# Optimization experiments

Hardware: AMD Instinct MI355X
Metric: run time of the kernel (lower is better)

## Reference

```python
import jax, jax.numpy as jnp
import numpy as np

# Model config (mirrors Mamba2Block(dim=256) with mamba_ssm defaults)
D_MODEL = 256
EXPAND = 2
D_INNER = D_MODEL * EXPAND          # 512
HEADDIM = D_MODEL * EXPAND // 8     # 64
NHEADS = D_INNER // HEADDIM         # 8
D_STATE = 64
D_CONV = 4
CONV_DIM = D_INNER + 2 * D_STATE    # 640 (ngroups=1)
D_IN_PROJ = 2 * D_INNER + 2 * D_STATE + NHEADS  # 1160
BATCH, SEQLEN = 2, 2048
EPS = 1e-5


def setup_inputs() -> dict:
    key = jax.random.key(0)
    ks = jax.random.split(key, 12)
    s = 0.02
    return {
        "hidden_states": jax.random.normal(ks[0], (BATCH, SEQLEN, D_MODEL), jnp.float32),
        "norm_w": jnp.ones((D_MODEL,), jnp.float32),
        "norm_b": jnp.zeros((D_MODEL,), jnp.float32),
        "W_in": jax.random.normal(ks[1], (D_MODEL, D_IN_PROJ), jnp.float32) * s,
        "conv_w": jax.random.normal(ks[2], (CONV_DIM, D_CONV), jnp.float32) * 0.25,
        "conv_b": jnp.zeros((CONV_DIM,), jnp.float32),
        "dt_bias": jax.random.uniform(ks[3], (NHEADS,), jnp.float32),
        "A_log": jax.random.uniform(ks[4], (NHEADS,), jnp.float32),  # A = -exp(A_log) in (-e, -1]
        "D_param": jnp.ones((NHEADS,), jnp.float32),
        "rms_w": jnp.ones((D_INNER,), jnp.float32),
        "W_out": jax.random.normal(ks[5], (D_INNER, D_MODEL), jnp.float32) * s,
    }


def _layer_norm(x, w, b):
    mu = jnp.mean(x, -1, keepdims=True)
    var = jnp.mean((x - mu) ** 2, -1, keepdims=True)
    return (x - mu) * jax.lax.rsqrt(var + EPS) * w + b


def _causal_depthwise_conv(x, w, b):
    # x: [B,L,C], w: [C,K] depthwise causal conv
    B, L, C = x.shape
    K = w.shape[1]
    xp = jnp.pad(x, ((0, 0), (K - 1, 0), (0, 0)))
    y = b
    for k in range(K):  # K=4, fixed small kernel
        y = y + w[:, k] * xp[:, k:k + L, :]
    return y


def reference(hidden_states, norm_w, norm_b, W_in, conv_w, conv_b, dt_bias, A_log, D_param, rms_w, W_out):
    B, L, D = hidden_states.shape
    residual = hidden_states                       # residual is None, drop_path=0
    x = _layer_norm(residual, norm_w, norm_b)      # pre-norm

    zxbcdt = jnp.einsum("bld,de->ble", x, W_in)    # [B,L,2*Di+2*N+H]
    z = zxbcdt[..., :D_INNER]
    xBC = zxbcdt[..., D_INNER:D_INNER + CONV_DIM]
    dt = zxbcdt[..., -NHEADS:]

    xBC = jax.nn.silu(_causal_depthwise_conv(xBC, conv_w, conv_b))
    xs = xBC[..., :D_INNER]
    Bm = xBC[..., D_INNER:D_INNER + D_STATE]       # [B,L,N] (ngroups=1)
    Cm = xBC[..., D_INNER + D_STATE:]              # [B,L,N]

    dt = jax.nn.softplus(dt + dt_bias)             # [B,L,H]
    A = -jnp.exp(A_log)                            # [H]
    dA = jnp.exp(dt * A)                           # [B,L,H]

    xh = xs.reshape(B, L, NHEADS, HEADDIM)         # [B,L,H,P]
    dtx = dt[..., None] * xh                       # [B,L,H,P]

    def step(s, inp):
        dA_t, dtx_t, B_t, C_t = inp                # [B,H],[B,H,P],[B,N],[B,N]
        s = s * dA_t[:, :, None, None] + dtx_t[..., None] * B_t[:, None, None, :]
        y_t = jnp.einsum("bhpn,bn->bhp", s, C_t)
        return s, y_t

    s0 = jnp.zeros((B, NHEADS, HEADDIM, D_STATE), hidden_states.dtype)
    xs_in = (jnp.swapaxes(dA, 0, 1), jnp.swapaxes(dtx, 0, 1),
             jnp.swapaxes(Bm, 0, 1), jnp.swapaxes(Cm, 0, 1))
    _, ys = jax.lax.scan(step, s0, xs_in)          # ys: [L,B,H,P]
    y = jnp.swapaxes(ys, 0, 1) + D_param[None, None, :, None] * xh  # skip term
    y = y.reshape(B, L, D_INNER)

    # gated RMSNorm (norm_before_gate=False): rmsnorm(y * silu(z)) * rms_w
    g = y * jax.nn.silu(z)
    g = g * jax.lax.rsqrt(jnp.mean(g * g, -1, keepdims=True) + EPS) * rms_w

    out = jnp.einsum("bld,de->ble", g, W_out)
    return out, residual
```

## Files before the change

### kernel.cpp

```cpp
#include <hip/hip_runtime.h>
#include <hip/hip_bf16.h>

#define BATCH 2
#define SEQLEN 2048
#define DMODEL 256
#define DINNER 512
#define NHEADS 8
#define HEADDIM 64
#define DSTATE 64
#define CONVDIM 640
#define DINPROJ 1160
#define NTOK (BATCH*SEQLEN)
#define Q 64
#define NCH (SEQLEN/Q)
#define NPAD_IN 1216
#define TS 72

typedef short v8s __attribute__((ext_vector_type(8)));
typedef float v4f __attribute__((ext_vector_type(4)));

__device__ __forceinline__ unsigned short f2bf(float f){
    __hip_bfloat16 h = __float2bfloat16(f);
    return *reinterpret_cast<unsigned short*>(&h);
}
__device__ __forceinline__ float bf2f(unsigned short u){
    unsigned int x = ((unsigned int)u) << 16;
    return __uint_as_float(x);
}

__global__ __launch_bounds__(256) void k_prep(
        const float* __restrict__ hid, const float* __restrict__ nw, const float* __restrict__ nb,
        const float* __restrict__ Win, const float* __restrict__ Wout,
        float* __restrict__ res, unsigned short* __restrict__ Xb,
        unsigned short* __restrict__ Wti, unsigned short* __restrict__ Wto){
    int bx = blockIdx.x;
    int t = threadIdx.x;
    if(bx < 256){
        __shared__ float xs[16][DMODEL];
        int tok0 = bx*16;
        for(int i=0;i<16;i++){
            int idx = i*256+t; int j = idx>>8, c = idx&255;
            float v = hid[(size_t)(tok0+j)*DMODEL + c];
            xs[j][c] = v;
            res[(size_t)(tok0+j)*DMODEL + c] = v;
        }
        __syncthreads();
        int g = t>>4, il = t&15;
        float sum=0.f, sumsq=0.f;
        for(int i=0;i<16;i++){ float v = xs[g][il*16+i]; sum += v; sumsq += v*v; }
        #pragma unroll
        for(int m=1;m<16;m<<=1){ sum += __shfl_xor(sum,m); sumsq += __shfl_xor(sumsq,m); }
        float mu   = sum*(1.f/256.f);
        float var  = sumsq*(1.f/256.f) - mu*mu;
        float rstd = rsqrtf(var + 1e-5f);
        for(int i=0;i<16;i++){
            int c = il*16+i;
            xs[g][c] = (xs[g][c]-mu)*rstd*nw[c] + nb[c];
        }
        __syncthreads();
        for(int i=0;i<16;i++){
            int idx = i*256+t; int j = idx>>8, c = idx&255;
            Xb[(size_t)(tok0+j)*DMODEL + c] = f2bf(xs[j][c]);
        }
    } else if(bx < 256 + NPAD_IN/4){
        int n0 = (bx-256)*4, k = t;
        #pragma unroll
        for(int i=0;i<4;i++){
            int n = n0+i;
            float v = (n < DINPROJ) ? Win[(size_t)k*DINPROJ + n] : 0.f;
            Wti[(size_t)n*DMODEL + k] = f2bf(v);
        }
    } else {
        int n0 = (bx - 256 - NPAD_IN/4)*4;
        #pragma unroll
        for(int kk=0;kk<2;kk++){
            int k = t + kk*256;
            #pragma unroll
            for(int i=0;i<4;i++){
                int n = n0+i;
                Wto[(size_t)n*DINNER + k] = f2bf(Wout[(size_t)k*DMODEL + n]);
            }
        }
    }
}

template<int BF16OUT>
__global__ __launch_bounds__(256) void k_gemm(
        const unsigned short* __restrict__ A, const unsigned short* __restrict__ Bt,
        float* __restrict__ Cf, unsigned short* __restrict__ Cb, int K, int Ncols){
    __shared__ __align__(16) unsigned short As[128*40];
    __shared__ __align__(16) unsigned short Bs[64*40];
    int t = threadIdx.x;
    int lane = t & 63, w = t >> 6;
    int lanelow = lane & 15, quad = lane >> 4;
    int tok0 = blockIdx.x * 128;
    int n0   = blockIdx.y * 64;
    v4f acc[2][4];
    #pragma unroll
    for(int mi=0;mi<2;mi++)
        #pragma unroll
        for(int ni=0;ni<4;ni++)
            acc[mi][ni] = (v4f){0.f,0.f,0.f,0.f};
    for(int k0=0; k0<K; k0+=32){
        __syncthreads();
        #pragma unroll
        for(int cc=0; cc<2; cc++){
            int c = t + cc*256;
            int row = c>>2, off = c&3;
            uint4 v = *(const uint4*)(A + (size_t)(tok0+row)*K + k0 + off*8);
            *(uint4*)&As[row*40 + off*8] = v;
        }
        {
            int row = t>>2, off = t&3;
            uint4 v = *(const uint4*)(Bt + (size_t)(n0+row)*K + k0 + off*8);
            *(uint4*)&Bs[row*40 + off*8] = v;
        }
        __syncthreads();
        v8s a0 = *(const v8s*)&As[(w*32 +      lanelow)*40 + quad*8];
        v8s a1 = *(const v8s*)&As[(w*32 + 16 + lanelow)*40 + quad*8];
        v8s b[4];
        #pragma unroll
        for(int ni=0;ni<4;ni++)
            b[ni] = *(const v8s*)&Bs[(ni*16 + lanelow)*40 + quad*8];
        #pragma unroll
        for(int ni=0;ni<4;ni++){
            acc[0][ni] = __builtin_amdgcn_mfma_f32_16x16x32_bf16(a0, b[ni], acc[0][ni], 0,0,0);
            acc[1][ni] = __builtin_amdgcn_mfma_f32_16x16x32_bf16(a1, b[ni], acc[1][ni], 0,0,0);
        }
    }
    #pragma unroll
    for(int mi=0;mi<2;mi++){
        #pragma unroll
        for(int ni=0;ni<4;ni++){
            int col = n0 + ni*16 + lanelow;
            if(col < Ncols){
                #pragma unroll
                for(int r=0;r<4;r++){
                    int row = tok0 + w*32 + mi*16 + quad*4 + r;
                    if(BF16OUT) Cb[(size_t)row*Ncols + col] = f2bf(acc[mi][ni][r]);
                    else        Cf[(size_t)row*Ncols + col] = acc[mi][ni][r];
                }
            }
        }
    }
}

__global__ __launch_bounds__(256) void k_chunk1(
        const unsigned short* __restrict__ zxb, const float* __restrict__ conv_w, const float* __restrict__ conv_b,
        const float* __restrict__ dt_bias, const float* __restrict__ A_log, const float* __restrict__ D_param,
        unsigned short* __restrict__ yw16, float* __restrict__ contrib,
        float* __restrict__ Larr, float* __restrict__ decayArr, unsigned short* __restrict__ Ccv){
    int blk = blockIdx.x;
    int c = blk & 31, h = (blk>>5)&7, b = blk>>8;
    int t = threadIdx.x;
    int lane = t & 63, w = t >> 6;
    int lanelow = lane & 15, quad = lane >> 4;
    __shared__ __align__(16) unsigned short Cb[64*TS];
    __shared__ __align__(16) unsigned short Bb[64*TS];
    __shared__ __align__(16) unsigned short BtW[64*TS];
    __shared__ __align__(16) unsigned short Xt[64*TS];
    __shared__ __align__(16) unsigned short Gbuf[64*TS];
    __shared__ float Ls[Q], dts[Q], wch[Q];
    int l0 = c*Q;
    int bh = b*NHEADS + h;
    const unsigned short* zbase = zxb + (size_t)(b*SEQLEN + l0)*DINPROJ;
    if(t < Q){
        float v = bf2f(zbase[(size_t)t*DINPROJ + (DINPROJ-NHEADS) + h]) + dt_bias[h];
        float dt = (v > 20.f) ? v : log1pf(__expf(v));
        float A  = -__expf(A_log[h]);
        float ld = dt*A;
        #pragma unroll
        for(int off=1; off<64; off<<=1){
            float u = __shfl_up(ld, off);
            if(lane >= off) ld += u;
        }
        Ls[t] = ld; dts[t] = dt;
    }
    __syncthreads();
    float L63 = Ls[Q-1];
    if(t < Q) wch[t] = __expf(L63 - Ls[t]) * dts[t];
    __syncthreads();
    unsigned short* CcP = Ccv + ((size_t)b*NCH + c)*4096;
    for(int i=0;i<12;i++){
        int u = t + 256*i;
        int st = u & 63, c4 = u >> 6, ch = c4*4;
        int gcol = (ch < 64) ? (DINNER + h*HEADDIM + ch) : (2*DINNER + (ch-64));
        const unsigned short* colp = zbase + (ptrdiff_t)st*DINPROJ + gcol;
        float xk[4][4];
        #pragma unroll
        for(int k=0;k<4;k++){
            int l = l0 + st + k - 3;
            ushort4 v;
            if(l >= 0) v = *(const ushort4*)(colp - (ptrdiff_t)(3-k)*DINPROJ);
            else { v.x=0; v.y=0; v.z=0; v.w=0; }
            xk[k][0]=bf2f(v.x); xk[k][1]=bf2f(v.y); xk[k][2]=bf2f(v.z); xk[k][3]=bf2f(v.w);
        }
        float wst = wch[st];
        #pragma unroll
        for(int j=0;j<4;j++){
            int chj = ch+j;
            int cc = (chj<64) ? (h*HEADDIM + chj) : (448 + chj);
            float4 wv = *(const float4*)&conv_w[cc*4];
            float acc = conv_b[cc] + wv.x*xk[0][j] + wv.y*xk[1][j] + wv.z*xk[2][j] + wv.w*xk[3][j];
            float sv = acc/(1.f+__expf(-acc));
            if(chj < 64){
                Xt[chj*TS + st] = f2bf(sv);
            } else if(chj < 128){
                int n = chj-64;
                Bb[st*TS + n]  = f2bf(sv);
                BtW[n*TS + st] = f2bf(sv*wst);
            } else {
                int n = chj-128;
                unsigned short sb = f2bf(sv);
                Cb[st*TS + n] = sb;
                if(h==0) CcP[st*64 + n] = sb;
            }
        }
    }
    __syncthreads();
    v4f g[4];
    #pragma unroll
    for(int nt=0;nt<4;nt++) g[nt] = (v4f){0.f,0.f,0.f,0.f};
    #pragma unroll
    for(int kk=0;kk<2;kk++){
        v8s a = *(const v8s*)&Cb[(w*16+lanelow)*TS + kk*32 + quad*8];
        #pragma unroll
        for(int nt=0;nt<4;nt++){
            v8s bb = *(const v8s*)&Bb[(nt*16+lanelow)*TS + kk*32 + quad*8];
            g[nt] = __builtin_amdgcn_mfma_f32_16x16x32_bf16(a, bb, g[nt], 0,0,0);
        }
    }
    float Lrow[4];
    #pragma unroll
    for(int r=0;r<4;r++) Lrow[r] = Ls[w*16 + quad*4 + r];
    #pragma unroll
    for(int nt=0;nt<4;nt++){
        int col = nt*16 + lanelow;
        float Lc = Ls[col], dtc = dts[col];
        #pragma unroll
        for(int r=0;r<4;r++){
            int rowg = w*16 + quad*4 + r;
            float val = (col <= rowg) ? g[nt][r] * __expf(Lrow[r]-Lc) * dtc : 0.f;
            Gbuf[rowg*TS + col] = f2bf(val);
        }
    }
    __syncthreads();
    v4f ya[4], sa[4];
    #pragma unroll
    for(int nt=0;nt<4;nt++){ ya[nt]=(v4f){0.f,0.f,0.f,0.f}; sa[nt]=(v4f){0.f,0.f,0.f,0.f}; }
    #pragma unroll
    for(int kk=0;kk<2;kk++){
        v8s ag = *(const v8s*)&Gbuf[(w*16+lanelow)*TS + kk*32 + quad*8];
        v8s ax = *(const v8s*)&Xt[(w*16+lanelow)*TS + kk*32 + quad*8];
        #pragma unroll
        for(int nt=0;nt<4;nt++){
            v8s bx = *(const v8s*)&Xt[(nt*16+lanelow)*TS + kk*32 + quad*8];
            v8s bw = *(const v8s*)&BtW[(nt*16+lanelow)*TS + kk*32 + quad*8];
            ya[nt] = __builtin_amdgcn_mfma_f32_16x16x32_bf16(ag, bx, ya[nt], 0,0,0);
            sa[nt] = __builtin_amdgcn_mfma_f32_16x16x32_bf16(ax, bw, sa[nt], 0,0,0);
        }
    }
    float Dp = D_param[h];
    #pragma unroll
    for(int nt=0;nt<4;nt++){
        int col = nt*16 + lanelow;
        #pragma unroll
        for(int r=0;r<4;r++){
            int i = w*16 + quad*4 + r;
            float xval = bf2f(Xt[col*TS + i]);
            yw16[((size_t)b*SEQLEN + l0 + i)*DINNER + h*HEADDIM + col] = f2bf(ya[nt][r] + Dp*xval);
            contrib[(((size_t)bh*NCH + c)*64 + i)*64 + col] = sa[nt][r];
        }
    }
    if(t < Q) Larr[((size_t)bh*NCH + c)*Q + t] = Ls[t];
    if(t == 0) decayArr[bh*NCH + c] = __expf(L63);
}

__global__ __launch_bounds__(256) void k_chunk2(const float* __restrict__ contrib,
                                                const float* __restrict__ decayArr,
                                                unsigned short* __restrict__ Sb){
    int bh = blockIdx.x >> 4;
    int part = blockIdx.x & 15;
    int e = part*256 + threadIdx.x;
    const size_t base = (size_t)bh*NCH*4096 + e;
    float vals[NCH];
    #pragma unroll
    for(int c=0;c<NCH;c++) vals[c] = contrib[base + (size_t)c*4096];
    float s = 0.f;
    #pragma unroll
    for(int c=0;c<NCH;c++){
        Sb[base + (size_t)c*4096] = f2bf(s);
        s = fmaf(s, decayArr[bh*NCH + c], vals[c]);
    }
}

__global__ __launch_bounds__(512) void k_tail(
        const unsigned short* __restrict__ Ccv, const unsigned short* __restrict__ Sb,
        const float* __restrict__ Larr, const unsigned short* __restrict__ yw16,
        const unsigned short* __restrict__ zxb, const float* __restrict__ rms_w,
        unsigned short* __restrict__ Gb){
    int blk = blockIdx.x;
    int half = blk & 1, c = (blk>>1) & 31, b = blk >> 6;
    int t = threadIdx.x;
    int h = t >> 6, lane = t & 63;
    int lanelow = lane & 15, quad = lane >> 4;
    int bh = b*NHEADS + h;
    __shared__ float wsum[8][32];
    __shared__ float rstdS[32];
    const unsigned short* Cp = Ccv + ((size_t)b*NCH + c)*4096;
    const unsigned short* Sp = Sb + ((size_t)bh*NCH + c)*4096;
    v8s a[2][2];
    #pragma unroll
    for(int rt=0;rt<2;rt++){
        int row = half*32 + rt*16 + lanelow;
        a[rt][0] = *(const v8s*)(Cp + row*64 + quad*8);
        a[rt][1] = *(const v8s*)(Cp + row*64 + 32 + quad*8);
    }
    v8s s[4][2];
    #pragma unroll
    for(int nt=0;nt<4;nt++){
        s[nt][0] = *(const v8s*)(Sp + (nt*16+lanelow)*64 + quad*8);
        s[nt][1] = *(const v8s*)(Sp + (nt*16+lanelow)*64 + 32 + quad*8);
    }
    float g[2][4][4];
    float sq[2][4];
    const float* Lp = Larr + ((size_t)bh*NCH + c)*Q;
    #pragma unroll
    for(int rt=0;rt<2;rt++){
        float eL[4];
        #pragma unroll
        for(int r=0;r<4;r++) eL[r] = __expf(Lp[half*32 + rt*16 + quad*4 + r]);
        #pragma unroll
        for(int nt=0;nt<4;nt++){
            v4f acc = (v4f){0.f,0.f,0.f,0.f};
            acc = __builtin_amdgcn_mfma_f32_16x16x32_bf16(a[rt][0], s[nt][0], acc, 0,0,0);
            acc = __builtin_amdgcn_mfma_f32_16x16x32_bf16(a[rt][1], s[nt][1], acc, 0,0,0);
            int col = h*HEADDIM + nt*16 + lanelow;
            #pragma unroll
            for(int r=0;r<4;r++){
                int i = half*32 + rt*16 + quad*4 + r;
                size_t tok = (size_t)b*SEQLEN + c*Q + i;
                float yv = acc[r]*eL[r] + bf2f(yw16[tok*DINNER + col]);
                float z  = bf2f(zxb[tok*DINPROJ + col]);
                float gg = yv * (z/(1.f+__expf(-z)));
                g[rt][nt][r] = gg;
                sq[rt][r] = (nt==0 ? gg*gg : sq[rt][r] + gg*gg);
            }
        }
    }
    #pragma unroll
    for(int rt=0;rt<2;rt++)
        #pragma unroll
        for(int r=0;r<4;r++){
            float v = sq[rt][r];
            #pragma unroll
            for(int m=1;m<16;m<<=1) v += __shfl_xor(v, m);
            sq[rt][r] = v;
        }
    if(lanelow==0){
        #pragma unroll
        for(int rt=0;rt<2;rt++)
            #pragma unroll
            for(int r=0;r<4;r++)
                wsum[h][rt*16 + quad*4 + r] = sq[rt][r];
    }
    __syncthreads();
    if(t < 32){
        float tot = 0.f;
        #pragma unroll
        for(int hh=0;hh<8;hh++) tot += wsum[hh][t];
        rstdS[t] = rsqrtf(tot*(1.f/512.f) + 1e-5f);
    }
    __syncthreads();
    #pragma unroll
    for(int rt=0;rt<2;rt++){
        #pragma unroll
        for(int nt=0;nt<4;nt++){
            int col = h*HEADDIM + nt*16 + lanelow;
            float rw = rms_w[col];
            #pragma unroll
            for(int r=0;r<4;r++){
                int i = rt*16 + quad*4 + r;
                Gb[((size_t)b*SEQLEN + c*Q + half*32 + i)*DINNER + col] = f2bf(g[rt][nt][r] * rstdS[i] * rw);
            }
        }
    }
}

extern "C" void kernel_launch(void* const* d_in, const int* in_sizes, int n_in,
                              void* d_out, int out_size, void* d_ws, size_t ws_size,
                              hipStream_t stream) {
    const float* hid     = (const float*)d_in[0];
    const float* norm_w  = (const float*)d_in[1];
    const float* norm_b  = (const float*)d_in[2];
    const float* Win     = (const float*)d_in[3];
    const float* conv_w  = (const float*)d_in[4];
    const float* conv_b  = (const float*)d_in[5];
    const float* dt_bias = (const float*)d_in[6];
    const float* A_log   = (const float*)d_in[7];
    const float* D_param = (const float*)d_in[8];
    const float* rms_w   = (const float*)d_in[9];
    const float* Wout    = (const float*)d_in[10];

    float* ws = (float*)d_ws;
    float* contrib = ws;
    float* Larr    = contrib + (size_t)16*NCH*4096;
    float* decayA  = Larr + (size_t)16*NCH*Q;
    unsigned short* zxb  = (unsigned short*)(decayA + 512);
    unsigned short* yw16 = zxb + (size_t)NTOK*DINPROJ;
    unsigned short* Sb   = yw16 + (size_t)NTOK*DINNER;
    unsigned short* Ccv  = Sb + (size_t)16*NCH*4096;
    unsigned short* Xb   = Ccv + (size_t)BATCH*NCH*4096;
    unsigned short* Gb   = Xb + (size_t)NTOK*DMODEL;
    unsigned short* Wti  = Gb + (size_t)NTOK*DINNER;
    unsigned short* Wto  = Wti + (size_t)NPAD_IN*DMODEL;

    float* out = (float*)d_out;
    float* res = out + (size_t)NTOK*DMODEL;

    k_prep<<<256 + NPAD_IN/4 + DMODEL/4, 256, 0, stream>>>(hid, norm_w, norm_b, Win, Wout, res, Xb, Wti, Wto);
    k_gemm<1><<<dim3(NTOK/128, NPAD_IN/64), 256, 0, stream>>>(Xb, Wti, nullptr, zxb, DMODEL, DINPROJ);
    k_chunk1<<<BATCH*NHEADS*NCH, 256, 0, stream>>>(zxb, conv_w, conv_b, dt_bias, A_log, D_param,
                                                   yw16, contrib, Larr, decayA, Ccv);
    k_chunk2<<<256, 256, 0, stream>>>(contrib, decayA, Sb);
    k_tail<<<BATCH*NCH*2, 512, 0, stream>>>(Ccv, Sb, Larr, yw16, zxb, rms_w, Gb);
    k_gemm<0><<<dim3(NTOK/128, DMODEL/64), 256, 0, stream>>>(Gb, Wto, out, nullptr, DINNER, DMODEL);
}
```

Before: 146.3 us.

## Fuse all stages into one persistent kernel with grid-wide atomic barriers

Merges the six kernel launches (prep, in-proj GEMM, chunk scan, inter-chunk recurrence, tail, out-proj GEMM) into one persistent 512-block kernel. Stages are separated by software grid barriers built on atomic counters. The tail now also fuses the gated RMSNorm with the output projection GEMM, folding rms_w into the transposed Wout and dropping the Gb intermediate. This removes launch gaps and one global round trip. The cost is spin-wait barriers, which require all 512 blocks to be co-resident, plus lower per-stage occupancy from the shared-memory union.

```diff
diff --git a/kernel.cpp b/kernel.cpp
--- a/kernel.cpp
+++ b/kernel.cpp
@@ -15,6 +15,7 @@
 #define NCH (SEQLEN/Q)
 #define NPAD_IN 1216
 #define TS 72
+#define NBLK 512
 
 typedef short v8s __attribute__((ext_vector_type(8)));
 typedef float v4f __attribute__((ext_vector_type(4)));
@@ -28,361 +29,364 @@
     return __uint_as_float(x);
 }
 
-__global__ __launch_bounds__(256) void k_prep(
+__device__ __forceinline__ void gbar(unsigned* sync, int idx){
+    __syncthreads();
+    if(threadIdx.x==0){
+        __threadfence();
+        atomicAdd(&sync[idx*16], 1u);
+        while(__hip_atomic_load(&sync[idx*16], __ATOMIC_RELAXED, __HIP_MEMORY_SCOPE_AGENT) < (unsigned)NBLK)
+            __builtin_amdgcn_s_sleep(8);
+        __threadfence();
+    }
+    __syncthreads();
+}
+
+__global__ __launch_bounds__(256, 2) void k_mega(
         const float* __restrict__ hid, const float* __restrict__ nw, const float* __restrict__ nb,
-        const float* __restrict__ Win, const float* __restrict__ Wout,
-        float* __restrict__ res, unsigned short* __restrict__ Xb,
-        unsigned short* __restrict__ Wti, unsigned short* __restrict__ Wto){
-    int bx = blockIdx.x;
+        const float* __restrict__ Win, const float* __restrict__ conv_w, const float* __restrict__ conv_b,
+        const float* __restrict__ dt_bias, const float* __restrict__ A_log, const float* __restrict__ D_param,
+        const float* __restrict__ rms_w, const float* __restrict__ Wout,
+        unsigned* __restrict__ sync,
+        float* __restrict__ contrib, float* __restrict__ Larr, float* __restrict__ decayA,
+        unsigned short* __restrict__ zxb, unsigned short* __restrict__ yw16,
+        unsigned short* __restrict__ Sb, unsigned short* __restrict__ Ccv,
+        unsigned short* __restrict__ Xb, unsigned short* __restrict__ Wti, unsigned short* __restrict__ Wto,
+        float* __restrict__ out, float* __restrict__ res){
+    int bid = blockIdx.x;
     int t = threadIdx.x;
-    if(bx < 256){
-        __shared__ float xs[16][DMODEL];
-        int tok0 = bx*16;
+    int lane = t & 63, w = t >> 6;
+    int lanelow = lane & 15, quad = lane >> 4;
+
+    __shared__ __align__(16) union SM {
+        struct { float xs[16][DMODEL]; } a;
+        struct { unsigned short As[128*40]; unsigned short Bs[64*40]; } b;
+        struct { unsigned short Cb[64*TS], Bb[64*TS], BtW[64*TS], Xt[64*TS], Gbuf[64*TS];
+                 float Ls[Q], dts[Q], wch[Q]; } c;
+        struct { unsigned short G[16*528]; float wsum[4][16]; float rstd[16]; } e;
+    } sm;
+
+    if(bid < 256){
+        int tok0 = bid*16;
         for(int i=0;i<16;i++){
-            int idx = i*256+t; int j = idx>>8, c = idx&255;
-            float v = hid[(size_t)(tok0+j)*DMODEL + c];
-            xs[j][c] = v;
-            res[(size_t)(tok0+j)*DMODEL + c] = v;
+            int idx = i*256+t; int j = idx>>8, cc = idx&255;
+            float v = hid[(size_t)(tok0+j)*DMODEL + cc];
+            sm.a.xs[j][cc] = v;
+            res[(size_t)(tok0+j)*DMODEL + cc] = v;
         }
         __syncthreads();
         int g = t>>4, il = t&15;
         float sum=0.f, sumsq=0.f;
-        for(int i=0;i<16;i++){ float v = xs[g][il*16+i]; sum += v; sumsq += v*v; }
+        for(int i=0;i<16;i++){ float v = sm.a.xs[g][il*16+i]; sum += v; sumsq += v*v; }
         #pragma unroll
         for(int m=1;m<16;m<<=1){ sum += __shfl_xor(sum,m); sumsq += __shfl_xor(sumsq,m); }
         float mu   = sum*(1.f/256.f);
         float var  = sumsq*(1.f/256.f) - mu*mu;
         float rstd = rsqrtf(var + 1e-5f);
         for(int i=0;i<16;i++){
-            int c = il*16+i;
-            xs[g][c] = (xs[g][c]-mu)*rstd*nw[c] + nb[c];
+            int cc = il*16+i;
+            sm.a.xs[g][cc] = (sm.a.xs[g][cc]-mu)*rstd*nw[cc] + nb[cc];
         }
         __syncthreads();
         for(int i=0;i<16;i++){
-            int idx = i*256+t; int j = idx>>8, c = idx&255;
-            Xb[(size_t)(tok0+j)*DMODEL + c] = f2bf(xs[j][c]);
-        }
-    } else if(bx < 256 + NPAD_IN/4){
-        int n0 = (bx-256)*4, k = t;
-        #pragma unroll
-        for(int i=0;i<4;i++){
-            int n = n0+i;
-            float v = (n < DINPROJ) ? Win[(size_t)k*DINPROJ + n] : 0.f;
-            Wti[(size_t)n*DMODEL + k] = f2bf(v);
-        }
-    } else {
-        int n0 = (bx - 256 - NPAD_IN/4)*4;
-        #pragma unroll
-        for(int kk=0;kk<2;kk++){
-            int k = t + kk*256;
+            int idx = i*256+t; int j = idx>>8, cc = idx&255;
+            Xb[(size_t)(tok0+j)*DMODEL + cc] = f2bf(sm.a.xs[j][cc]);
+        }
+    }
+    if(bid >= 144){
+        int u = bid - 144;
+        if(u < 304){
+            int n0 = u*4, k = t;
             #pragma unroll
             for(int i=0;i<4;i++){
                 int n = n0+i;
-                Wto[(size_t)n*DINNER + k] = f2bf(Wout[(size_t)k*DMODEL + n]);
-            }
-        }
-    }
-}
-
-template<int BF16OUT>
-__global__ __launch_bounds__(256) void k_gemm(
-        const unsigned short* __restrict__ A, const unsigned short* __restrict__ Bt,
-        float* __restrict__ Cf, unsigned short* __restrict__ Cb, int K, int Ncols){
-    __shared__ __align__(16) unsigned short As[128*40];
-    __shared__ __align__(16) unsigned short Bs[64*40];
-    int t = threadIdx.x;
-    int lane = t & 63, w = t >> 6;
-    int lanelow = lane & 15, quad = lane >> 4;
-    int tok0 = blockIdx.x * 128;
-    int n0   = blockIdx.y * 64;
-    v4f acc[2][4];
-    #pragma unroll
-    for(int mi=0;mi<2;mi++)
-        #pragma unroll
-        for(int ni=0;ni<4;ni++)
-            acc[mi][ni] = (v4f){0.f,0.f,0.f,0.f};
-    for(int k0=0; k0<K; k0+=32){
-        __syncthreads();
-        #pragma unroll
-        for(int cc=0; cc<2; cc++){
-            int c = t + cc*256;
-            int row = c>>2, off = c&3;
-            uint4 v = *(const uint4*)(A + (size_t)(tok0+row)*K + k0 + off*8);
-            *(uint4*)&As[row*40 + off*8] = v;
-        }
-        {
-            int row = t>>2, off = t&3;
-            uint4 v = *(const uint4*)(Bt + (size_t)(n0+row)*K + k0 + off*8);
-            *(uint4*)&Bs[row*40 + off*8] = v;
-        }
-        __syncthreads();
-        v8s a0 = *(const v8s*)&As[(w*32 +      lanelow)*40 + quad*8];
-        v8s a1 = *(const v8s*)&As[(w*32 + 16 + lanelow)*40 + quad*8];
-        v8s b[4];
-        #pragma unroll
-        for(int ni=0;ni<4;ni++)
-            b[ni] = *(const v8s*)&Bs[(ni*16 + lanelow)*40 + quad*8];
-        #pragma unroll
-        for(int ni=0;ni<4;ni++){
-            acc[0][ni] = __builtin_amdgcn_mfma_f32_16x16x32_bf16(a0, b[ni], acc[0][ni], 0,0,0);
-            acc[1][ni] = __builtin_amdgcn_mfma_f32_16x16x32_bf16(a1, b[ni], acc[1][ni], 0,0,0);
-        }
-    }
-    #pragma unroll
-    for(int mi=0;mi<2;mi++){
-        #pragma unroll
-        for(int ni=0;ni<4;ni++){
-            int col = n0 + ni*16 + lanelow;
-            if(col < Ncols){
+                float v = (n < DINPROJ) ? Win[(size_t)k*DINPROJ + n] : 0.f;
+                Wti[(size_t)n*DMODEL + k] = f2bf(v);
+            }
+        } else {
+            int n0 = (u-304)*4;
+            #pragma unroll
+            for(int kk=0;kk<2;kk++){
+                int k = t + kk*256;
+                float rw = rms_w[k];
+                #pragma unroll
+                for(int i=0;i<4;i++){
+                    int n = n0+i;
+                    Wto[(size_t)n*DINNER + k] = f2bf(Wout[(size_t)k*DMODEL + n] * rw);
+                }
+            }
+        }
+    }
+    gbar(sync, 0);
+
+    for(int u = bid; u < 608; u += NBLK){
+        int tok0 = (u & 31) * 128;
+        int n0   = (u >> 5) * 64;
+        v4f acc[2][4];
+        #pragma unroll
+        for(int mi=0;mi<2;mi++)
+            #pragma unroll
+            for(int ni=0;ni<4;ni++)
+                acc[mi][ni] = (v4f){0.f,0.f,0.f,0.f};
+        for(int k0=0; k0<DMODEL; k0+=32){
+            __syncthreads();
+            #pragma unroll
+            for(int cc=0; cc<2; cc++){
+                int c = t + cc*256;
+                int row = c>>2, off = c&3;
+                uint4 v = *(const uint4*)(Xb + (size_t)(tok0+row)*DMODEL + k0 + off*8);
+                *(uint4*)&sm.b.As[row*40 + off*8] = v;
+            }
+            {
+                int row = t>>2, off = t&3;
+                uint4 v = *(const uint4*)(Wti + (size_t)(n0+row)*DMODEL + k0 + off*8);
+                *(uint4*)&sm.b.Bs[row*40 + off*8] = v;
+            }
+            __syncthreads();
+            v8s a0 = *(const v8s*)&sm.b.As[(w*32 +      lanelow)*40 + quad*8];
+            v8s a1 = *(const v8s*)&sm.b.As[(w*32 + 16 + lanelow)*40 + quad*8];
+            v8s b[4];
+            #pragma unroll
+            for(int ni=0;ni<4;ni++)
+                b[ni] = *(const v8s*)&sm.b.Bs[(ni*16 + lanelow)*40 + quad*8];
+            #pragma unroll
+            for(int ni=0;ni<4;ni++){
+                acc[0][ni] = __builtin_amdgcn_mfma_f32_16x16x32_bf16(a0, b[ni], acc[0][ni], 0,0,0);
+                acc[1][ni] = __builtin_amdgcn_mfma_f32_16x16x32_bf16(a1, b[ni], acc[1][ni], 0,0,0);
+            }
+        }
+        #pragma unroll
+        for(int mi=0;mi<2;mi++){
+            #pragma unroll
+            for(int ni=0;ni<4;ni++){
+                int col = n0 + ni*16 + lanelow;
+                if(col < DINPROJ){
+                    #pragma unroll
+                    for(int r=0;r<4;r++){
+                        int row = tok0 + w*32 + mi*16 + quad*4 + r;
+                        zxb[(size_t)row*DINPROJ + col] = f2bf(acc[mi][ni][r]);
+                    }
+                }
+            }
+        }
+        __syncthreads();
+    }
+    gbar(sync, 1);
+
+    {
+        int c = bid & 31, h = (bid>>5)&7, b = bid>>8;
+        int l0 = c*Q;
+        int bh = b*NHEADS + h;
+        const unsigned short* zbase = zxb + (size_t)(b*SEQLEN + l0)*DINPROJ;
+        if(t < Q){
+            float v = bf2f(zbase[(size_t)t*DINPROJ + (DINPROJ-NHEADS) + h]) + dt_bias[h];
+            float dt = (v > 20.f) ? v : log1pf(__expf(v));
+            float A  = -__expf(A_log[h]);
+            float ld = dt*A;
+            #pragma unroll
+            for(int off=1; off<64; off<<=1){
+                float u = __shfl_up(ld, off);
+                if(lane >= off) ld += u;
+            }
+            sm.c.Ls[t] = ld; sm.c.dts[t] = dt;
+        }
+        __syncthreads();
+        float L63 = sm.c.Ls[Q-1];
+        if(t < Q) sm.c.wch[t] = __expf(L63 - sm.c.Ls[t]) * sm.c.dts[t];
+        __syncthreads();
+        unsigned short* CcP = Ccv + ((size_t)b*NCH + c)*4096;
+        for(int i=0;i<12;i++){
+            int u = t + 256*i;
+            int st = u & 63, c4 = u >> 6, ch = c4*4;
+            int gcol = (ch < 64) ? (DINNER + h*HEADDIM + ch) : (2*DINNER + (ch-64));
+            const unsigned short* colp = zbase + (ptrdiff_t)st*DINPROJ + gcol;
+            float xk[4][4];
+            #pragma unroll
+            for(int k=0;k<4;k++){
+                int l = l0 + st + k - 3;
+                ushort4 v;
+                if(l >= 0) v = *(const ushort4*)(colp - (ptrdiff_t)(3-k)*DINPROJ);
+                else { v.x=0; v.y=0; v.z=0; v.w=0; }
+                xk[k][0]=bf2f(v.x); xk[k][1]=bf2f(v.y); xk[k][2]=bf2f(v.z); xk[k][3]=bf2f(v.w);
+            }
+            float wst = sm.c.wch[st];
+            #pragma unroll
+            for(int j=0;j<4;j++){
+                int chj = ch+j;
+                int cc = (chj<64) ? (h*HEADDIM + chj) : (448 + chj);
+                float4 wv = *(const float4*)&conv_w[cc*4];
+                float acc = conv_b[cc] + wv.x*xk[0][j] + wv.y*xk[1][j] + wv.z*xk[2][j] + wv.w*xk[3][j];
+                float sv = acc/(1.f+__expf(-acc));
+                if(chj < 64){
+                    sm.c.Xt[chj*TS + st] = f2bf(sv);
+                } else if(chj < 128){
+                    int n = chj-64;
+                    sm.c.Bb[st*TS + n]  = f2bf(sv);
+                    sm.c.BtW[n*TS + st] = f2bf(sv*wst);
+                } else {
+                    int n = chj-128;
+                    unsigned short sb16 = f2bf(sv);
+                    sm.c.Cb[st*TS + n] = sb16;
+                    if(h==0) CcP[st*64 + n] = sb16;
+                }
+            }
+        }
+        __syncthreads();
+        v4f g[4];
+        #pragma unroll
+        for(int nt=0;nt<4;nt++) g[nt] = (v4f){0.f,0.f,0.f,0.f};
+        #pragma unroll
+        for(int kk=0;kk<2;kk++){
+            v8s a = *(const v8s*)&sm.c.Cb[(w*16+lanelow)*TS + kk*32 + quad*8];
+            #pragma unroll
+            for(int nt=0;nt<4;nt++){
+                v8s bb = *(const v8s*)&sm.c.Bb[(nt*16+lanelow)*TS + kk*32 + quad*8];
+                g[nt] = __builtin_amdgcn_mfma_f32_16x16x32_bf16(a, bb, g[nt], 0,0,0);
+            }
+        }
+        float Lrow[4];
+        #pragma unroll
+        for(int r=0;r<4;r++) Lrow[r] = sm.c.Ls[w*16 + quad*4 + r];
+        #pragma unroll
+        for(int nt=0;nt<4;nt++){
+            int col = nt*16 + lanelow;
+            float Lc = sm.c.Ls[col], dtc = sm.c.dts[col];
+            #pragma unroll
+            for(int r=0;r<4;r++){
+                int rowg = w*16 + quad*4 + r;
+                float val = (col <= rowg) ? g[nt][r] * __expf(Lrow[r]-Lc) * dtc : 0.f;
+                sm.c.Gbuf[rowg*TS + col] = f2bf(val);
+            }
+        }
+        __syncthreads();
+        v4f ya[4], sa[4];
+        #pragma unroll
+        for(int nt=0;nt<4;nt++){ ya[nt]=(v4f){0.f,0.f,0.f,0.f}; sa[nt]=(v4f){0.f,0.f,0.f,0.f}; }
+        #pragma unroll
+        for(int kk=0;kk<2;kk++){
+            v8s ag = *(const v8s*)&sm.c.Gbuf[(w*16+lanelow)*TS + kk*32 + quad*8];
+            v8s ax = *(const v8s*)&sm.c.Xt[(w*16+lanelow)*TS + kk*32 + quad*8];
+            #pragma unroll
+            for(int nt=0;nt<4;nt++){
+                v8s bx = *(const v8s*)&sm.c.Xt[(nt*16+lanelow)*TS + kk*32 + quad*8];
+                v8s bw = *(const v8s*)&sm.c.BtW[(nt*16+lanelow)*TS + kk*32 + quad*8];
+                ya[nt] = __builtin_amdgcn_mfma_f32_16x16x32_bf16(ag, bx, ya[nt], 0,0,0);
+                sa[nt] = __builtin_amdgcn_mfma_f32_16x16x32_bf16(ax, bw, sa[nt], 0,0,0);
+            }
+        }
+        float Dp = D_param[h];
+        #pragma unroll
+        for(int nt=0;nt<4;nt++){
+            int col = nt*16 + lanelow;
+            #pragma unroll
+            for(int r=0;r<4;r++){
+                int i = w*16 + quad*4 + r;
+                float xval = bf2f(sm.c.Xt[col*TS + i]);
+                yw16[((size_t)b*SEQLEN + l0 + i)*DINNER + h*HEADDIM + col] = f2bf(ya[nt][r] + Dp*xval);
+                contrib[(((size_t)bh*NCH + c)*64 + i)*64 + col] = sa[nt][r];
+            }
+        }
+        if(t < Q) Larr[((size_t)bh*NCH + c)*Q + t] = sm.c.Ls[t];
+        if(t == 0) decayA[bh*NCH + c] = __expf(L63);
+    }
+    gbar(sync, 2);
+
+    if(t < 128){
+        int eg = bid*128 + t;
+        int bh = eg >> 12;
+        int e  = eg & 4095;
+        const size_t base = (size_t)bh*NCH*4096 + e;
+        float vals[NCH];
+        #pragma unroll
+        for(int c=0;c<NCH;c++) vals[c] = contrib[base + (size_t)c*4096];
+        float s = 0.f;
+        #pragma unroll
+        for(int c=0;c<NCH;c++){
+            Sb[base + (size_t)c*4096] = f2bf(s);
+            s = fmaf(s, decayA[bh*NCH + c], vals[c]);
+        }
+    }
+    gbar(sync, 3);
+
+    if(bid < 256){
+        int b = bid >> 7, tg = bid & 127;
+        int c = tg >> 2, q16 = tg & 3;
+        size_t tok0 = (size_t)b*SEQLEN + c*Q + q16*16;
+        float gg[2][4][4];
+        float sq[4] = {0.f,0.f,0.f,0.f};
+        const unsigned short* Cp = Ccv + ((size_t)b*NCH + c)*4096;
+        #pragma unroll
+        for(int hh=0; hh<2; hh++){
+            int h = w*2 + hh;
+            int bh = b*NHEADS + h;
+            const unsigned short* Sp = Sb + ((size_t)bh*NCH + c)*4096;
+            const float* Lp = Larr + ((size_t)bh*NCH + c)*Q;
+            v8s a0 = *(const v8s*)(Cp + (q16*16+lanelow)*64 + quad*8);
+            v8s a1 = *(const v8s*)(Cp + (q16*16+lanelow)*64 + 32 + quad*8);
+            float eL[4];
+            #pragma unroll
+            for(int r=0;r<4;r++) eL[r] = __expf(Lp[q16*16 + quad*4 + r]);
+            #pragma unroll
+            for(int nt=0;nt<4;nt++){
+                v8s s0 = *(const v8s*)(Sp + (nt*16+lanelow)*64 + quad*8);
+                v8s s1 = *(const v8s*)(Sp + (nt*16+lanelow)*64 + 32 + quad*8);
+                v4f acc = (v4f){0.f,0.f,0.f,0.f};
+                acc = __builtin_amdgcn_mfma_f32_16x16x32_bf16(a0, s0, acc, 0,0,0);
+                acc = __builtin_amdgcn_mfma_f32_16x16x32_bf16(a1, s1, acc, 0,0,0);
+                int col = h*HEADDIM + nt*16 + lanelow;
                 #pragma unroll
                 for(int r=0;r<4;r++){
-                    int row = tok0 + w*32 + mi*16 + quad*4 + r;
-                    if(BF16OUT) Cb[(size_t)row*Ncols + col] = f2bf(acc[mi][ni][r]);
-                    else        Cf[(size_t)row*Ncols + col] = acc[mi][ni][r];
+                    int i = quad*4 + r;
+                    size_t tok = tok0 + i;
+                    float yv = acc[r]*eL[r] + bf2f(yw16[tok*DINNER + col]);
+                    float z  = bf2f(zxb[tok*DINPROJ + col]);
+                    float gv = yv * (z/(1.f+__expf(-z)));
+                    gg[hh][nt][r] = gv;
+                    sq[r] += gv*gv;
                 }
             }
         }
-    }
-}
-
-__global__ __launch_bounds__(256) void k_chunk1(
-        const unsigned short* __restrict__ zxb, const float* __restrict__ conv_w, const float* __restrict__ conv_b,
-        const float* __restrict__ dt_bias, const float* __restrict__ A_log, const float* __restrict__ D_param,
-        unsigned short* __restrict__ yw16, float* __restrict__ contrib,
-        float* __restrict__ Larr, float* __restrict__ decayArr, unsigned short* __restrict__ Ccv){
-    int blk = blockIdx.x;
-    int c = blk & 31, h = (blk>>5)&7, b = blk>>8;
-    int t = threadIdx.x;
-    int lane = t & 63, w = t >> 6;
-    int lanelow = lane & 15, quad = lane >> 4;
-    __shared__ __align__(16) unsigned short Cb[64*TS];
-    __shared__ __align__(16) unsigned short Bb[64*TS];
-    __shared__ __align__(16) unsigned short BtW[64*TS];
-    __shared__ __align__(16) unsigned short Xt[64*TS];
-    __shared__ __align__(16) unsigned short Gbuf[64*TS];
-    __shared__ float Ls[Q], dts[Q], wch[Q];
-    int l0 = c*Q;
-    int bh = b*NHEADS + h;
-    const unsigned short* zbase = zxb + (size_t)(b*SEQLEN + l0)*DINPROJ;
-    if(t < Q){
-        float v = bf2f(zbase[(size_t)t*DINPROJ + (DINPROJ-NHEADS) + h]) + dt_bias[h];
-        float dt = (v > 20.f) ? v : log1pf(__expf(v));
-        float A  = -__expf(A_log[h]);
-        float ld = dt*A;
-        #pragma unroll
-        for(int off=1; off<64; off<<=1){
-            float u = __shfl_up(ld, off);
-            if(lane >= off) ld += u;
-        }
-        Ls[t] = ld; dts[t] = dt;
-    }
-    __syncthreads();
-    float L63 = Ls[Q-1];
-    if(t < Q) wch[t] = __expf(L63 - Ls[t]) * dts[t];
-    __syncthreads();
-    unsigned short* CcP = Ccv + ((size_t)b*NCH + c)*4096;
-    for(int i=0;i<12;i++){
-        int u = t + 256*i;
-        int st = u & 63, c4 = u >> 6, ch = c4*4;
-        int gcol = (ch < 64) ? (DINNER + h*HEADDIM + ch) : (2*DINNER + (ch-64));
-        const unsigned short* colp = zbase + (ptrdiff_t)st*DINPROJ + gcol;
-        float xk[4][4];
-        #pragma unroll
-        for(int k=0;k<4;k++){
-            int l = l0 + st + k - 3;
-            ushort4 v;
-            if(l >= 0) v = *(const ushort4*)(colp - (ptrdiff_t)(3-k)*DINPROJ);
-            else { v.x=0; v.y=0; v.z=0; v.w=0; }
-            xk[k][0]=bf2f(v.x); xk[k][1]=bf2f(v.y); xk[k][2]=bf2f(v.z); xk[k][3]=bf2f(v.w);
-        }
-        float wst = wch[st];
-        #pragma unroll
-        for(int j=0;j<4;j++){
-            int chj = ch+j;
-            int cc = (chj<64) ? (h*HEADDIM + chj) : (448 + chj);
-            float4 wv = *(const float4*)&conv_w[cc*4];
-            float acc = conv_b[cc] + wv.x*xk[0][j] + wv.y*xk[1][j] + wv.z*xk[2][j] + wv.w*xk[3][j];
-            float sv = acc/(1.f+__expf(-acc));
-            if(chj < 64){
-                Xt[chj*TS + st] = f2bf(sv);
-            } else if(chj < 128){
-                int n = chj-64;
-                Bb[st*TS + n]  = f2bf(sv);
-                BtW[n*TS + st] = f2bf(sv*wst);
-            } else {
-                int n = chj-128;
-                unsigned short sb = f2bf(sv);
-                Cb[st*TS + n] = sb;
-                if(h==0) CcP[st*64 + n] = sb;
-            }
-        }
-    }
-    __syncthreads();
-    v4f g[4];
-    #pragma unroll
-    for(int nt=0;nt<4;nt++) g[nt] = (v4f){0.f,0.f,0.f,0.f};
-    #pragma unroll
-    for(int kk=0;kk<2;kk++){
-        v8s a = *(const v8s*)&Cb[(w*16+lanelow)*TS + kk*32 + quad*8];
+        #pragma unroll
+        for(int hh=0;hh<2;hh++)
+            #pragma unroll
+            for(int nt=0;nt<4;nt++)
+                #pragma unroll
+                for(int r=0;r<4;r++)
+                    sm.e.G[(quad*4+r)*528 + (w*2+hh)*64 + nt*16 + lanelow] = f2bf(gg[hh][nt][r]);
+        #pragma unroll
+        for(int r=0;r<4;r++){
+            float v = sq[r];
+            #pragma unroll
+            for(int m=1;m<16;m<<=1) v += __shfl_xor(v, m);
+            sq[r] = v;
+        }
+        if(lanelow==0){
+            #pragma unroll
+            for(int r=0;r<4;r++) sm.e.wsum[w][quad*4+r] = sq[r];
+        }
+        __syncthreads();
+        if(t < 16)
+            sm.e.rstd[t] = rsqrtf((sm.e.wsum[0][t]+sm.e.wsum[1][t]+sm.e.wsum[2][t]+sm.e.wsum[3][t])*(1.f/512.f) + 1e-5f);
+        __syncthreads();
+        v4f acc[4];
+        #pragma unroll
+        for(int nt=0;nt<4;nt++) acc[nt] = (v4f){0.f,0.f,0.f,0.f};
+        for(int ki=0; ki<16; ki++){
+            v8s a = *(const v8s*)&sm.e.G[lanelow*528 + ki*32 + quad*8];
+            #pragma unroll
+            for(int nt=0;nt<4;nt++){
+                v8s bfr = *(const v8s*)(Wto + (size_t)(w*64 + nt*16 + lanelow)*DINNER + ki*32 + quad*8);
+                acc[nt] = __builtin_amdgcn_mfma_f32_16x16x32_bf16(a, bfr, acc[nt], 0,0,0);
+            }
+        }
+        float rs[4];
+        #pragma unroll
+        for(int r=0;r<4;r++) rs[r] = sm.e.rstd[quad*4+r];
         #pragma unroll
         for(int nt=0;nt<4;nt++){
-            v8s bb = *(const v8s*)&Bb[(nt*16+lanelow)*TS + kk*32 + quad*8];
-            g[nt] = __builtin_amdgcn_mfma_f32_16x16x32_bf16(a, bb, g[nt], 0,0,0);
-        }
-    }
-    float Lrow[4];
-    #pragma unroll
-    for(int r=0;r<4;r++) Lrow[r] = Ls[w*16 + quad*4 + r];
-    #pragma unroll
-    for(int nt=0;nt<4;nt++){
-        int col = nt*16 + lanelow;
-        float Lc = Ls[col], dtc = dts[col];
-        #pragma unroll
-        for(int r=0;r<4;r++){
-            int rowg = w*16 + quad*4 + r;
-            float val = (col <= rowg) ? g[nt][r] * __expf(Lrow[r]-Lc) * dtc : 0.f;
-            Gbuf[rowg*TS + col] = f2bf(val);
-        }
-    }
-    __syncthreads();
-    v4f ya[4], sa[4];
-    #pragma unroll
-    for(int nt=0;nt<4;nt++){ ya[nt]=(v4f){0.f,0.f,0.f,0.f}; sa[nt]=(v4f){0.f,0.f,0.f,0.f}; }
-    #pragma unroll
-    for(int kk=0;kk<2;kk++){
-        v8s ag = *(const v8s*)&Gbuf[(w*16+lanelow)*TS + kk*32 + quad*8];
-        v8s ax = *(const v8s*)&Xt[(w*16+lanelow)*TS + kk*32 + quad*8];
-        #pragma unroll
-        for(int nt=0;nt<4;nt++){
-            v8s bx = *(const v8s*)&Xt[(nt*16+lanelow)*TS + kk*32 + quad*8];
-            v8s bw = *(const v8s*)&BtW[(nt*16+lanelow)*TS + kk*32 + quad*8];
-            ya[nt] = __builtin_amdgcn_mfma_f32_16x16x32_bf16(ag, bx, ya[nt], 0,0,0);
-            sa[nt] = __builtin_amdgcn_mfma_f32_16x16x32_bf16(ax, bw, sa[nt], 0,0,0);
-        }
-    }
-    float Dp = D_param[h];
-    #pragma unroll
-    for(int nt=0;nt<4;nt++){
-        int col = nt*16 + lanelow;
-        #pragma unroll
-        for(int r=0;r<4;r++){
-            int i = w*16 + quad*4 + r;
-            float xval = bf2f(Xt[col*TS + i]);
-            yw16[((size_t)b*SEQLEN + l0 + i)*DINNER + h*HEADDIM + col] = f2bf(ya[nt][r] + Dp*xval);
-            contrib[(((size_t)bh*NCH + c)*64 + i)*64 + col] = sa[nt][r];
-        }
-    }
-    if(t < Q) Larr[((size_t)bh*NCH + c)*Q + t] = Ls[t];
-    if(t == 0) decayArr[bh*NCH + c] = __expf(L63);
-}
-
-__global__ __launch_bounds__(256) void k_chunk2(const float* __restrict__ contrib,
-                                                const float* __restrict__ decayArr,
-                                                unsigned short* __restrict__ Sb){
-    int bh = blockIdx.x >> 4;
-    int part = blockIdx.x & 15;
-    int e = part*256 + threadIdx.x;
-    const size_t base = (size_t)bh*NCH*4096 + e;
-    float vals[NCH];
-    #pragma unroll
-    for(int c=0;c<NCH;c++) vals[c] = contrib[base + (size_t)c*4096];
-    float s = 0.f;
-    #pragma unroll
-    for(int c=0;c<NCH;c++){
-        Sb[base + (size_t)c*4096] = f2bf(s);
-        s = fmaf(s, decayArr[bh*NCH + c], vals[c]);
-    }
-}
-
-__global__ __launch_bounds__(512) void k_tail(
-        const unsigned short* __restrict__ Ccv, const unsigned short* __restrict__ Sb,
-        const float* __restrict__ Larr, const unsigned short* __restrict__ yw16,
-        const unsigned short* __restrict__ zxb, const float* __restrict__ rms_w,
-        unsigned short* __restrict__ Gb){
-    int blk = blockIdx.x;
-    int half = blk & 1, c = (blk>>1) & 31, b = blk >> 6;
-    int t = threadIdx.x;
-    int h = t >> 6, lane = t & 63;
-    int lanelow = lane & 15, quad = lane >> 4;
-    int bh = b*NHEADS + h;
-    __shared__ float wsum[8][32];
-    __shared__ float rstdS[32];
-    const unsigned short* Cp = Ccv + ((size_t)b*NCH + c)*4096;
-    const unsigned short* Sp = Sb + ((size_t)bh*NCH + c)*4096;
-    v8s a[2][2];
-    #pragma unroll
-    for(int rt=0;rt<2;rt++){
-        int row = half*32 + rt*16 + lanelow;
-        a[rt][0] = *(const v8s*)(Cp + row*64 + quad*8);
-        a[rt][1] = *(const v8s*)(Cp + row*64 + 32 + quad*8);
-    }
-    v8s s[4][2];
-    #pragma unroll
-    for(int nt=0;nt<4;nt++){
-        s[nt][0] = *(const v8s*)(Sp + (nt*16+lanelow)*64 + quad*8);
-        s[nt][1] = *(const v8s*)(Sp + (nt*16+lanelow)*64 + 32 + quad*8);
-    }
-    float g[2][4][4];
-    float sq[2][4];
-    const float* Lp = Larr + ((size_t)bh*NCH + c)*Q;
-    #pragma unroll
-    for(int rt=0;rt<2;rt++){
-        float eL[4];
-        #pragma unroll
-        for(int r=0;r<4;r++) eL[r] = __expf(Lp[half*32 + rt*16 + quad*4 + r]);
-        #pragma unroll
-        for(int nt=0;nt<4;nt++){
-            v4f acc = (v4f){0.f,0.f,0.f,0.f};
-            acc = __builtin_amdgcn_mfma_f32_16x16x32_bf16(a[rt][0], s[nt][0], acc, 0,0,0);
-            acc = __builtin_amdgcn_mfma_f32_16x16x32_bf16(a[rt][1], s[nt][1], acc, 0,0,0);
-            int col = h*HEADDIM + nt*16 + lanelow;
-            #pragma unroll
-            for(int r=0;r<4;r++){
-                int i = half*32 + rt*16 + quad*4 + r;
-                size_t tok = (size_t)b*SEQLEN + c*Q + i;
-                float yv = acc[r]*eL[r] + bf2f(yw16[tok*DINNER + col]);
-                float z  = bf2f(zxb[tok*DINPROJ + col]);
-                float gg = yv * (z/(1.f+__expf(-z)));
-                g[rt][nt][r] = gg;
-                sq[rt][r] = (nt==0 ? gg*gg : sq[rt][r] + gg*gg);
-            }
-        }
-    }
-    #pragma unroll
-    for(int rt=0;rt<2;rt++)
-        #pragma unroll
-        for(int r=0;r<4;r++){
-            float v = sq[rt][r];
-            #pragma unroll
-            for(int m=1;m<16;m<<=1) v += __shfl_xor(v, m);
-            sq[rt][r] = v;
-        }
-    if(lanelow==0){
-        #pragma unroll
-        for(int rt=0;rt<2;rt++)
+            int col = w*64 + nt*16 + lanelow;
             #pragma unroll
             for(int r=0;r<4;r++)
-                wsum[h][rt*16 + quad*4 + r] = sq[rt][r];
-    }
-    __syncthreads();
-    if(t < 32){
-        float tot = 0.f;
-        #pragma unroll
-        for(int hh=0;hh<8;hh++) tot += wsum[hh][t];
-        rstdS[t] = rsqrtf(tot*(1.f/512.f) + 1e-5f);
-    }
-    __syncthreads();
-    #pragma unroll
-    for(int rt=0;rt<2;rt++){
-        #pragma unroll
-        for(int nt=0;nt<4;nt++){
-            int col = h*HEADDIM + nt*16 + lanelow;
-            float rw = rms_w[col];
-            #pragma unroll
-            for(int r=0;r<4;r++){
-                int i = rt*16 + quad*4 + r;
-                Gb[((size_t)b*SEQLEN + c*Q + half*32 + i)*DINNER + col] = f2bf(g[rt][nt][r] * rstdS[i] * rw);
-            }
+                out[(tok0 + quad*4 + r)*DMODEL + col] = acc[nt][r]*rs[r];
         }
     }
 }
@@ -402,8 +406,8 @@
     const float* rms_w   = (const float*)d_in[9];
     const float* Wout    = (const float*)d_in[10];
 
-    float* ws = (float*)d_ws;
-    float* contrib = ws;
+    unsigned* sync = (unsigned*)d_ws;
+    float* contrib = (float*)d_ws + 256;
     float* Larr    = contrib + (size_t)16*NCH*4096;
     float* decayA  = Larr + (size_t)16*NCH*Q;
     unsigned short* zxb  = (unsigned short*)(decayA + 512);
@@ -411,18 +415,15 @@
     unsigned short* Sb   = yw16 + (size_t)NTOK*DINNER;
     unsigned short* Ccv  = Sb + (size_t)16*NCH*4096;
     unsigned short* Xb   = Ccv + (size_t)BATCH*NCH*4096;
-    unsigned short* Gb   = Xb + (size_t)NTOK*DMODEL;
-    unsigned short* Wti  = Gb + (size_t)NTOK*DINNER;
+    unsigned short* Wti  = Xb + (size_t)NTOK*DMODEL;
     unsigned short* Wto  = Wti + (size_t)NPAD_IN*DMODEL;
 
     float* out = (float*)d_out;
     float* res = out + (size_t)NTOK*DMODEL;
 
-    k_prep<<<256 + NPAD_IN/4 + DMODEL/4, 256, 0, stream>>>(hid, norm_w, norm_b, Win, Wout, res, Xb, Wti, Wto);
-    k_gemm<1><<<dim3(NTOK/128, NPAD_IN/64), 256, 0, stream>>>(Xb, Wti, nullptr, zxb, DMODEL, DINPROJ);
-    k_chunk1<<<BATCH*NHEADS*NCH, 256, 0, stream>>>(zxb, conv_w, conv_b, dt_bias, A_log, D_param,
-                                                   yw16, contrib, Larr, decayA, Ccv);
-    k_chunk2<<<256, 256, 0, stream>>>(contrib, decayA, Sb);
-    k_tail<<<BATCH*NCH*2, 512, 0, stream>>>(Ccv, Sb, Larr, yw16, zxb, rms_w, Gb);
-    k_gemm<0><<<dim3(NTOK/128, DMODEL/64), 256, 0, stream>>>(Gb, Wto, out, nullptr, DINNER, DMODEL);
+    hipMemsetAsync(sync, 0, 4*16*sizeof(unsigned), stream);
+    k_mega<<<NBLK, 256, 0, stream>>>(hid, norm_w, norm_b, Win, conv_w, conv_b,
+                                     dt_bias, A_log, D_param, rms_w, Wout,
+                                     sync, contrib, Larr, decayA, zxb, yw16, Sb, Ccv,
+                                     Xb, Wti, Wto, out, res);
 }
```

Measured after the change: 362.7 us. 148% more time.

## Stage conv inputs through shared memory and store chunk state contributions in bf16

Applied to the files above, without the earlier changes.

The depthwise-conv stage in k_chunk1 now loads each input row once into a shared-memory staging buffer, in four 16-token slabs, and the conv reads its 4 taps from LDS. Before, every output re-read its 4 taps from global memory. Separately, the per-chunk state contributions passed from k_chunk1 to k_chunk2 are stored as bf16 instead of fp32, halving that intermediate traffic. The cost is extra barriers per slab and reduced precision in the inter-chunk state recurrence inputs.

```diff
diff --git a/kernel.cpp b/kernel.cpp
--- a/kernel.cpp
+++ b/kernel.cpp
@@ -15,6 +15,7 @@
 #define NCH (SEQLEN/Q)
 #define NPAD_IN 1216
 #define TS 72
+#define RS3 196
 
 typedef short v8s __attribute__((ext_vector_type(8)));
 typedef float v4f __attribute__((ext_vector_type(4)));
@@ -148,7 +149,7 @@
 __global__ __launch_bounds__(256) void k_chunk1(
         const unsigned short* __restrict__ zxb, const float* __restrict__ conv_w, const float* __restrict__ conv_b,
         const float* __restrict__ dt_bias, const float* __restrict__ A_log, const float* __restrict__ D_param,
-        unsigned short* __restrict__ yw16, float* __restrict__ contrib,
+        unsigned short* __restrict__ yw16, unsigned short* __restrict__ contrib16,
         float* __restrict__ Larr, float* __restrict__ decayArr, unsigned short* __restrict__ Ccv){
     int blk = blockIdx.x;
     int c = blk & 31, h = (blk>>5)&7, b = blk>>8;
@@ -160,6 +161,7 @@
     __shared__ __align__(16) unsigned short BtW[64*TS];
     __shared__ __align__(16) unsigned short Xt[64*TS];
     __shared__ __align__(16) unsigned short Gbuf[64*TS];
+    __shared__ __align__(16) unsigned short raw[19*RS3];
     __shared__ float Ls[Q], dts[Q], wch[Q];
     int l0 = c*Q;
     int bh = b*NHEADS + h;
@@ -179,41 +181,55 @@
     __syncthreads();
     float L63 = Ls[Q-1];
     if(t < Q) wch[t] = __expf(L63 - Ls[t]) * dts[t];
-    __syncthreads();
     unsigned short* CcP = Ccv + ((size_t)b*NCH + c)*4096;
-    for(int i=0;i<12;i++){
-        int u = t + 256*i;
-        int st = u & 63, c4 = u >> 6, ch = c4*4;
-        int gcol = (ch < 64) ? (DINNER + h*HEADDIM + ch) : (2*DINNER + (ch-64));
-        const unsigned short* colp = zbase + (ptrdiff_t)st*DINPROJ + gcol;
-        float xk[4][4];
-        #pragma unroll
-        for(int k=0;k<4;k++){
-            int l = l0 + st + k - 3;
-            ushort4 v;
-            if(l >= 0) v = *(const ushort4*)(colp - (ptrdiff_t)(3-k)*DINPROJ);
-            else { v.x=0; v.y=0; v.z=0; v.w=0; }
-            xk[k][0]=bf2f(v.x); xk[k][1]=bf2f(v.y); xk[k][2]=bf2f(v.z); xk[k][3]=bf2f(v.w);
-        }
-        float wst = wch[st];
-        #pragma unroll
-        for(int j=0;j<4;j++){
-            int chj = ch+j;
-            int cc = (chj<64) ? (h*HEADDIM + chj) : (448 + chj);
-            float4 wv = *(const float4*)&conv_w[cc*4];
-            float acc = conv_b[cc] + wv.x*xk[0][j] + wv.y*xk[1][j] + wv.z*xk[2][j] + wv.w*xk[3][j];
-            float sv = acc/(1.f+__expf(-acc));
-            if(chj < 64){
-                Xt[chj*TS + st] = f2bf(sv);
-            } else if(chj < 128){
-                int n = chj-64;
-                Bb[st*TS + n]  = f2bf(sv);
-                BtW[n*TS + st] = f2bf(sv*wst);
-            } else {
-                int n = chj-128;
-                unsigned short sb = f2bf(sv);
-                Cb[st*TS + n] = sb;
-                if(h==0) CcP[st*64 + n] = sb;
+    for(int s=0; s<4; s++){
+        __syncthreads();
+        #pragma unroll
+        for(int i=0;i<4;i++){
+            int u = t + 256*i;
+            if(u < 19*48){
+                int row = u/48, seg = u%48;
+                int l = l0 + s*16 - 3 + row;
+                int gcol = (seg<16) ? (DINNER + h*HEADDIM + seg*4) : (2*DINNER + (seg-16)*4);
+                ushort4 v;
+                if(l >= 0) v = *(const ushort4*)(zxb + ((size_t)b*SEQLEN + l)*DINPROJ + gcol);
+                else { v.x=0; v.y=0; v.z=0; v.w=0; }
+                *(ushort4*)&raw[row*RS3 + seg*4] = v;
+            }
+        }
+        __syncthreads();
+        #pragma unroll
+        for(int i=0;i<3;i++){
+            int u = t + 256*i;
+            int stl = u & 15, grp = u >> 4;
+            int st = s*16 + stl;
+            int ch = grp*4;
+            float xk[4][4];
+            #pragma unroll
+            for(int k=0;k<4;k++){
+                ushort4 v = *(const ushort4*)&raw[(stl+k)*RS3 + ch];
+                xk[k][0]=bf2f(v.x); xk[k][1]=bf2f(v.y); xk[k][2]=bf2f(v.z); xk[k][3]=bf2f(v.w);
+            }
+            float wst = wch[st];
+            #pragma unroll
+            for(int j=0;j<4;j++){
+                int chj = ch+j;
+                int cc = (chj<64) ? (h*HEADDIM + chj) : (448 + chj);
+                float4 wv = *(const float4*)&conv_w[cc*4];
+                float acc = conv_b[cc] + wv.x*xk[0][j] + wv.y*xk[1][j] + wv.z*xk[2][j] + wv.w*xk[3][j];
+                float sv = acc/(1.f+__expf(-acc));
+                if(chj < 64){
+                    Xt[chj*TS + st] = f2bf(sv);
+                } else if(chj < 128){
+                    int n = chj-64;
+                    Bb[st*TS + n]  = f2bf(sv);
+                    BtW[n*TS + st] = f2bf(sv*wst);
+                } else {
+                    int n = chj-128;
+                    unsigned short sb16 = f2bf(sv);
+                    Cb[st*TS + n] = sb16;
+                    if(h==0) CcP[st*64 + n] = sb16;
+                }
             }
         }
     }
@@ -269,14 +285,14 @@
             int i = w*16 + quad*4 + r;
             float xval = bf2f(Xt[col*TS + i]);
             yw16[((size_t)b*SEQLEN + l0 + i)*DINNER + h*HEADDIM + col] = f2bf(ya[nt][r] + Dp*xval);
-            contrib[(((size_t)bh*NCH + c)*64 + i)*64 + col] = sa[nt][r];
+            contrib16[(((size_t)bh*NCH + c)*64 + i)*64 + col] = f2bf(sa[nt][r]);
         }
     }
     if(t < Q) Larr[((size_t)bh*NCH + c)*Q + t] = Ls[t];
     if(t == 0) decayArr[bh*NCH + c] = __expf(L63);
 }
 
-__global__ __launch_bounds__(256) void k_chunk2(const float* __restrict__ contrib,
+__global__ __launch_bounds__(256) void k_chunk2(const unsigned short* __restrict__ contrib16,
                                                 const float* __restrict__ decayArr,
                                                 unsigned short* __restrict__ Sb){
     int bh = blockIdx.x >> 4;
@@ -285,7 +301,7 @@
     const size_t base = (size_t)bh*NCH*4096 + e;
     float vals[NCH];
     #pragma unroll
-    for(int c=0;c<NCH;c++) vals[c] = contrib[base + (size_t)c*4096];
+    for(int c=0;c<NCH;c++) vals[c] = bf2f(contrib16[base + (size_t)c*4096]);
     float s = 0.f;
     #pragma unroll
     for(int c=0;c<NCH;c++){
@@ -402,9 +418,8 @@
     const float* rms_w   = (const float*)d_in[9];
     const float* Wout    = (const float*)d_in[10];
 
-    float* ws = (float*)d_ws;
-    float* contrib = ws;
-    float* Larr    = contrib + (size_t)16*NCH*4096;
+    unsigned short* contrib16 = (unsigned short*)d_ws;
+    float* Larr    = (float*)(contrib16 + (size_t)16*NCH*4096);
     float* decayA  = Larr + (size_t)16*NCH*Q;
     unsigned short* zxb  = (unsigned short*)(decayA + 512);
     unsigned short* yw16 = zxb + (size_t)NTOK*DINPROJ;
@@ -421,8 +436,8 @@
     k_prep<<<256 + NPAD_IN/4 + DMODEL/4, 256, 0, stream>>>(hid, norm_w, norm_b, Win, Wout, res, Xb, Wti, Wto);
     k_gemm<1><<<dim3(NTOK/128, NPAD_IN/64), 256, 0, stream>>>(Xb, Wti, nullptr, zxb, DMODEL, DINPROJ);
     k_chunk1<<<BATCH*NHEADS*NCH, 256, 0, stream>>>(zxb, conv_w, conv_b, dt_bias, A_log, D_param,
-                                                   yw16, contrib, Larr, decayA, Ccv);
-    k_chunk2<<<256, 256, 0, stream>>>(contrib, decayA, Sb);
+                                                   yw16, contrib16, Larr, decayA, Ccv);
+    k_chunk2<<<256, 256, 0, stream>>>(contrib16, decayA, Sb);
     k_tail<<<BATCH*NCH*2, 512, 0, stream>>>(Ccv, Sb, Larr, yw16, zxb, rms_w, Gb);
     k_gemm<0><<<dim3(NTOK/128, DMODEL/64), 256, 0, stream>>>(Gb, Wto, out, nullptr, DINNER, DMODEL);
 }
```

Measured after the change: 138.8 us. 5.1% less time.
